# Kernel optimization log

Measured on AMD Instinct MI355X. Metric: run time of the kernel, lower is better.

Reference implementation:

```python
import jax, jax.numpy as jnp
import numpy as np

VOCAB, E, H, B, S, C = 200000, 256, 512, 32, 512, 2


def setup_inputs() -> dict:
    key = jax.random.key(0)
    ks = jax.random.split(key, 10)
    emb = jax.random.normal(ks[0], (VOCAB, E), jnp.float32) * 0.1
    # torch code appends a zero row used as pad_idx
    emb_table = jnp.concatenate([emb, jnp.zeros((1, E), jnp.float32)], axis=0)  # [VOCAB+1, E]
    x = jax.random.randint(ks[1], (B, S), -1, VOCAB, dtype=jnp.int32)  # -1 marks UNK tokens
    unk_vec = jax.random.normal(ks[2], (E,), jnp.float32)
    induction = jax.random.normal(ks[3], (E, E), jnp.float32) / np.float32(np.sqrt(E))
    s = np.float32(1.0 / np.sqrt(H))  # torch GRU default init: U(-1/sqrt(H), 1/sqrt(H))
    W_ih = jax.random.uniform(ks[4], (3 * H, E), jnp.float32, -s, s)
    W_hh = jax.random.uniform(ks[5], (3 * H, H), jnp.float32, -s, s)
    b_ih = jax.random.uniform(ks[6], (3 * H,), jnp.float32, -s, s)
    b_hh = jax.random.uniform(ks[7], (3 * H,), jnp.float32, -s, s)
    W_proj = jax.random.normal(ks[8], (C, H), jnp.float32) * np.float32(np.sqrt(2.0 / (C + H)))  # xavier normal
    b_proj = jnp.zeros((C,), jnp.float32)
    return dict(x=x, emb_table=emb_table, unk_vec=unk_vec, induction=induction,
                W_ih=W_ih, W_hh=W_hh, b_ih=b_ih, b_hh=b_hh, W_proj=W_proj, b_proj=b_proj)


def _gru(e, W_ih, W_hh, b_ih, b_hh):
    # e: [B,S,E] -> hidden states [B,S,H], torch GRU gate order (r, z, n)
    xi = jnp.einsum('bse,ge->bsg', e, W_ih) + b_ih  # precompute input gates, g = 3H
    h0 = jnp.zeros((e.shape[0], W_hh.shape[1]), e.dtype)

    def step(h, xt):
        gh = h @ W_hh.T + b_hh
        xr, xz, xn = jnp.split(xt, 3, axis=-1)
        hr, hz, hn = jnp.split(gh, 3, axis=-1)
        r = jax.nn.sigmoid(xr + hr)
        z = jax.nn.sigmoid(xz + hz)
        n = jnp.tanh(xn + r * hn)
        h_new = (1.0 - z) * n + z * h
        return h_new, h_new

    _, hs = jax.lax.scan(step, h0, jnp.swapaxes(xi, 0, 1))  # [S,B,H]
    return jnp.swapaxes(hs, 0, 1)


def reference(x, emb_table, unk_vec, induction, W_ih, W_hh, b_ih, b_hh, W_proj, b_proj):
    pad_idx = emb_table.shape[0] - 1
    unk = x == -1  # [B,S]
    tok = jnp.where(unk, pad_idx, x)
    e = emb_table[tok]  # [B,S,E] gather (memory-bound)
    # Faithful to induce_embeddings as written: context list is always empty (bug),
    # so every UNK position gets induction_matrix @ unk_vec.
    induced = induction @ unk_vec  # [E]
    e = jnp.where(unk[..., None], induced, e)
    h = _gru(e, W_ih, W_hh, b_ih, b_hh)  # [B,S,H]
    pooled = jnp.max(h, axis=1)  # torch.max(x, 1).values
    # dropout is identity at inference
    return pooled @ W_proj.T + b_proj  # [B,C]
```

## Files before the change

### kernel.cpp

```cpp
#include <hip/hip_runtime.h>
#include <hip/hip_bf16.h>

#define EDIM 256
#define HDIM 512
#define BB 32
#define SS 512
#define CC 2
#define G3 1536

typedef unsigned int u32;
typedef unsigned long long u64;
typedef __attribute__((ext_vector_type(8))) short short8;
typedef __attribute__((ext_vector_type(4))) float f32x4;

__device__ __forceinline__ float toF(float v) { return v; }
__device__ __forceinline__ float toF(__hip_bfloat16 v) { return __bfloat162float(v); }
__device__ __forceinline__ void storeX(float* p, float v) { *p = v; }
__device__ __forceinline__ void storeX(__hip_bfloat16* p, float v) { *p = __float2bfloat16(v); }

__device__ __forceinline__ unsigned short f2bf(float f) {
  u32 b = __float_as_uint(f);
  return (unsigned short)((b + 0x7FFFu + ((b >> 16) & 1u)) >> 16);
}

__global__ void k_init(const float* __restrict__ induction, const float* __restrict__ unk_vec,
                       float* __restrict__ induced, u64* __restrict__ thw) {
  const int t = threadIdx.x;
  const int wg = blockIdx.x;
  if (wg < 16) {
    u64* p = thw + (size_t)wg * 1024;
    for (int i = t; i < 1024; i += 256) p[i] = 0ull;
  } else {
    float acc = 0.f;
    const float* row = induction + t * EDIM;
#pragma unroll 4
    for (int j = 0; j < EDIM; j += 4) {
      float4 a = *(const float4*)(row + j);
      float4 u = *(const float4*)(unk_vec + j);
      acc += a.x * u.x + a.y * u.y + a.z * u.z + a.w * u.w;
    }
    induced[t] = acc;
  }
}

template <typename XT>
__global__ __launch_bounds__(256) void k_xi(const int* __restrict__ x, const float* __restrict__ emb,
                                            const float* __restrict__ induced,
                                            const float* __restrict__ W_ih, const float* __restrict__ b_ih,
                                            XT* __restrict__ xi) {
  __shared__ __align__(16) unsigned short As[128][40];
  __shared__ __align__(16) unsigned short Bs[128][40];
  __shared__ int toks[128];
  __shared__ float bcol[128];
  const int c0 = blockIdx.x * 128;
  const int r0 = blockIdx.y * 128;
  const int tid = threadIdx.x;
  if (tid < 128) { toks[tid] = x[r0 + tid]; bcol[tid] = b_ih[c0 + tid]; }
  __syncthreads();

  const int wv = tid >> 6, ln = tid & 63;
  const int lr = tid & 127, kh = tid >> 7;
  const int fm = ln & 15, fq = ln >> 4;

  f32x4 acc[2][8];
#pragma unroll
  for (int i = 0; i < 2; i++)
#pragma unroll
    for (int j = 0; j < 8; j++) acc[i][j] = (f32x4){0.f, 0.f, 0.f, 0.f};

  const int tok = toks[lr];
  const float* abase = (tok < 0 ? induced : emb + (size_t)tok * EDIM) + kh * 16;
  const float* bbase = W_ih + (size_t)(c0 + lr) * EDIM + kh * 16;

  for (int kk = 0; kk < EDIM; kk += 32) {
    unsigned short av[16], bv[16];
#pragma unroll
    for (int q = 0; q < 4; q++) {
      float4 ta = *(const float4*)(abase + kk + q * 4);
      float4 tb = *(const float4*)(bbase + kk + q * 4);
      av[q * 4 + 0] = f2bf(ta.x); av[q * 4 + 1] = f2bf(ta.y);
      av[q * 4 + 2] = f2bf(ta.z); av[q * 4 + 3] = f2bf(ta.w);
      bv[q * 4 + 0] = f2bf(tb.x); bv[q * 4 + 1] = f2bf(tb.y);
      bv[q * 4 + 2] = f2bf(tb.z); bv[q * 4 + 3] = f2bf(tb.w);
    }
    *(uint4*)&As[lr][kh * 16 + 0] = *(uint4*)&av[0];
    *(uint4*)&As[lr][kh * 16 + 8] = *(uint4*)&av[8];
    *(uint4*)&Bs[lr][kh * 16 + 0] = *(uint4*)&bv[0];
    *(uint4*)&Bs[lr][kh * 16 + 8] = *(uint4*)&bv[8];
    __syncthreads();

    short8 af0 = *(const short8*)&As[wv * 32 + fm][fq * 8];
    short8 af1 = *(const short8*)&As[wv * 32 + 16 + fm][fq * 8];
#pragma unroll
    for (int ni = 0; ni < 8; ni++) {
      short8 bf = *(const short8*)&Bs[ni * 16 + fm][fq * 8];
      acc[0][ni] = __builtin_amdgcn_mfma_f32_16x16x32_bf16(af0, bf, acc[0][ni], 0, 0, 0);
      acc[1][ni] = __builtin_amdgcn_mfma_f32_16x16x32_bf16(af1, bf, acc[1][ni], 0, 0, 0);
    }
    __syncthreads();
  }

#pragma unroll
  for (int mi = 0; mi < 2; mi++)
#pragma unroll
    for (int ni = 0; ni < 8; ni++) {
      const int col = c0 + ni * 16 + fm;
      const float bb = bcol[ni * 16 + fm];
#pragma unroll
      for (int r = 0; r < 4; r++) {
        const int row = r0 + wv * 32 + mi * 16 + fq * 4 + r;
        storeX(xi + (size_t)row * G3 + col, acc[mi][ni][r] + bb);
      }
    }
}

template <typename XT>
__global__ __launch_bounds__(256, 1) void k_gru(const XT* __restrict__ xi, const float* __restrict__ W_hh,
                                                const float* __restrict__ b_hh, u64* __restrict__ thw,
                                                float* __restrict__ pooled) {
  const int wg = blockIdx.x;
  const int g = wg & 7;
  const int m = wg >> 3;
  const int bbase = g * 4;
  const int i0 = m * 16;
  const int tid = threadIdx.x;
  const int iu = tid >> 4;
  const int ks = tid & 15;
  const int i = i0 + iu;
  const int swz = ks & 7;

  f32x4 w[3][8];
#pragma unroll
  for (int q = 0; q < 3; q++) {
    const float* wr = W_hh + (size_t)(q * HDIM + i) * HDIM + ks * 32;
#pragma unroll
    for (int j = 0; j < 8; j++) w[q][j] = *(const f32x4*)(wr + j * 4);
  }
  const float bh0 = b_hh[i], bh1 = b_hh[HDIM + i], bh2 = b_hh[2 * HDIM + i];

  const bool gate = (ks < 4);
  const int gb = ks & 3;
  const int hpIdx = ((((i >> 2) ^ ((i >> 5) & 7)) << 2) | (i & 3));
  const int foff = ((((tid >> 1) ^ ((tid >> 4) & 7)) << 2) | ((tid & 1) << 1));

  u64* slot = thw + (size_t)g * 2 * 1024;
  __shared__ __align__(16) float hs[2][4][512];

  float pmax = -3.0e38f;

  float cxr = 0.f, cxz = 0.f, cxn = 0.f;
  if (gate) {
    const size_t xo = (size_t)(bbase + gb) * SS * G3 + i;
    cxr = toF(xi[xo]); cxz = toF(xi[xo + HDIM]); cxn = toF(xi[xo + 2 * HDIM]);
  }

  for (int s = 0; s < SS; s++) {
    float nxr = 0.f, nxz = 0.f, nxn = 0.f;
    if (gate && s + 1 < SS) {
      const size_t xo = ((size_t)(bbase + gb) * SS + (s + 1)) * G3 + i;
      nxr = toF(xi[xo]); nxz = toF(xi[xo + HDIM]); nxn = toF(xi[xo + 2 * HDIM]);
    }

    float* hb = &hs[s & 1][0][0];
    if (s == 0) {
#pragma unroll
      for (int t = 0; t < 8; t++) hb[t * 256 + tid] = 0.f;
    } else {
      const u64* src = slot + (size_t)(s & 1) * 1024 + tid;
      const u32 need = (u32)s;
      u64 v[4];
#pragma unroll
      for (int j = 0; j < 4; j++)
        v[j] = __hip_atomic_load(src + j * 256, __ATOMIC_RELAXED, __HIP_MEMORY_SCOPE_AGENT);
      u32 pend = 0;
#pragma unroll
      for (int j = 0; j < 4; j++)
        if ((u32)(v[j] & 0xFFFFu) != need) pend |= 1u << j;
      int guard = 0;
      while (pend && guard < (1 << 20)) {
        __builtin_amdgcn_s_sleep(1);
#pragma unroll
        for (int j = 0; j < 4; j++)
          if (pend & (1u << j))
            v[j] = __hip_atomic_load(src + j * 256, __ATOMIC_RELAXED, __HIP_MEMORY_SCOPE_AGENT);
#pragma unroll
        for (int j = 0; j < 4; j++)
          if ((pend & (1u << j)) && (u32)(v[j] & 0xFFFFu) == need) pend &= ~(1u << j);
        guard++;
      }
#pragma unroll
      for (int j = 0; j < 4; j++) {
        const float a = __uint_as_float((u32)(v[j] >> 40) << 8);
        const float b = __uint_as_float((u32)((v[j] >> 16) & 0xFFFFFFu) << 8);
        *(float2*)&hb[j * 512 + foff] = make_float2(a, b);
      }
    }
    __syncthreads();

    f32x4 acc[4][3];
#pragma unroll
    for (int b = 0; b < 4; b++)
#pragma unroll
      for (int q = 0; q < 3; q++) acc[b][q] = (f32x4){0.f, 0.f, 0.f, 0.f};

#pragma unroll
    for (int b = 0; b < 4; b++) {
      const float* hr = hb + b * 512 + ks * 32;
#pragma unroll
      for (int j = 0; j < 8; j++) {
        const f32x4 hv = *(const f32x4*)(hr + ((j ^ swz) << 2));
        acc[b][0] = __builtin_elementwise_fma(w[0][j], hv, acc[b][0]);
        acc[b][1] = __builtin_elementwise_fma(w[1][j], hv, acc[b][1]);
        acc[b][2] = __builtin_elementwise_fma(w[2][j], hv, acc[b][2]);
      }
    }

    float ha[4][3];
#pragma unroll
    for (int b = 0; b < 4; b++)
#pragma unroll
      for (int q = 0; q < 3; q++) {
        const f32x4 t = acc[b][q];
        ha[b][q] = (t.x + t.y) + (t.z + t.w);
      }

    float v3[3];
#pragma unroll
    for (int q = 0; q < 3; q++) {
      const float s01 = (ks & 1) ? ha[0][q] : ha[1][q];
      const float r01 = __shfl_xor(s01, 1, 64);
      const float k01 = (ks & 1) ? ha[1][q] : ha[0][q];
      const float a01 = k01 + r01;
      const float s23 = (ks & 1) ? ha[2][q] : ha[3][q];
      const float r23 = __shfl_xor(s23, 1, 64);
      const float k23 = (ks & 1) ? ha[3][q] : ha[2][q];
      const float a23 = k23 + r23;
      const float s2 = (ks & 2) ? a01 : a23;
      const float r2 = __shfl_xor(s2, 2, 64);
      const float k2 = (ks & 2) ? a23 : a01;
      float t = k2 + r2;
      t += __shfl_xor(t, 4, 64);
      t += __shfl_xor(t, 8, 64);
      v3[q] = t;
    }

    if (gate) {
      const float hr_ = bh0 + v3[0];
      const float hz_ = bh1 + v3[1];
      const float hn_ = bh2 + v3[2];
      const float r = 1.f / (1.f + expf(-(cxr + hr_)));
      const float z = 1.f / (1.f + expf(-(cxz + hz_)));
      const float n = tanhf(cxn + r * hn_);
      const float hp = hb[gb * 512 + hpIdx];
      const float hnew = (1.f - z) * n + z * hp;
      pmax = fmaxf(pmax, hnew);
      const float pv = __shfl_xor(hnew, 16, 64);
      if (!(iu & 1)) {
        const u32 abits = ((__float_as_uint(hnew) + 0x80u) >> 8) & 0xFFFFFFu;
        const u32 bbits = ((__float_as_uint(pv) + 0x80u) >> 8) & 0xFFFFFFu;
        const u64 pkt = ((u64)abits << 40) | ((u64)bbits << 16) | (u64)(u32)(s + 1);
        const int W = gb * 256 + (i >> 1);
        __hip_atomic_store(slot + (size_t)((s + 1) & 1) * 1024 + W, pkt,
                           __ATOMIC_RELAXED, __HIP_MEMORY_SCOPE_AGENT);
      }
    }
    cxr = nxr; cxz = nxz; cxn = nxn;
  }

  if (gate) pooled[(size_t)(bbase + gb) * HDIM + i] = pmax;
}

__global__ void k_out(const float* __restrict__ pooled, const float* __restrict__ W_proj,
                      const float* __restrict__ b_proj, float* __restrict__ out) {
  const int t = threadIdx.x;
  const int b = t >> 1, c = t & 1;
  const float* p = pooled + (size_t)b * HDIM;
  const float* wr = W_proj + (size_t)c * HDIM;
  float acc = 0.f;
#pragma unroll 4
  for (int k = 0; k < HDIM; k += 4) {
    float4 pv = *(const float4*)(p + k);
    float4 wv = *(const float4*)(wr + k);
    acc += pv.x * wv.x + pv.y * wv.y + pv.z * wv.z + pv.w * wv.w;
  }
  out[b * CC + c] = acc + b_proj[c];
}

extern "C" void kernel_launch(void* const* d_in, const int* in_sizes, int n_in,
                              void* d_out, int out_size, void* d_ws, size_t ws_size,
                              hipStream_t stream) {
  const int* x = (const int*)d_in[0];
  const float* emb = (const float*)d_in[1];
  const float* unk = (const float*)d_in[2];
  const float* induction = (const float*)d_in[3];
  const float* W_ih = (const float*)d_in[4];
  const float* W_hh = (const float*)d_in[5];
  const float* b_ih = (const float*)d_in[6];
  const float* b_hh = (const float*)d_in[7];
  const float* W_proj = (const float*)d_in[8];
  const float* b_proj = (const float*)d_in[9];
  float* out = (float*)d_out;

  const size_t xi_f32 = (size_t)BB * SS * G3 * 4;
  const size_t xi_b16 = (size_t)BB * SS * G3 * 2;
  const size_t thw_sz = (size_t)8 * 2 * 1024 * 8;
  const size_t tail = thw_sz + (size_t)BB * HDIM * 4 + EDIM * 4 + 4096;
  const bool usef32 = ws_size >= xi_f32 + tail;

  char* p = (char*)d_ws;
  void* xi = p;
  p += ((usef32 ? xi_f32 : xi_b16) + 255) & ~(size_t)255;
  u64* thw = (u64*)p;         p += thw_sz;
  float* pooled = (float*)p;  p += (size_t)BB * HDIM * 4;
  float* induced = (float*)p;

  k_init<<<17, 256, 0, stream>>>(induction, unk, induced, thw);
  if (usef32) {
    k_xi<float><<<dim3(12, 128), 256, 0, stream>>>(x, emb, induced, W_ih, b_ih, (float*)xi);
    k_gru<float><<<256, 256, 0, stream>>>((const float*)xi, W_hh, b_hh, thw, pooled);
  } else {
    k_xi<__hip_bfloat16><<<dim3(12, 128), 256, 0, stream>>>(x, emb, induced, W_ih, b_ih,
                                                            (__hip_bfloat16*)xi);
    k_gru<__hip_bfloat16><<<256, 256, 0, stream>>>((const __hip_bfloat16*)xi, W_hh, b_hh, thw, pooled);
  }
  k_out<<<1, 64, 0, stream>>>(pooled, W_proj, b_proj, out);
}
```

Baseline: 1.781 ms.

## Split each GRU step into two batch-pair phases to overlap cross-workgroup waits

Each workgroup's four batch rows are processed as two pairs per timestep. Each pair waits only on its own two slots of the previous hidden state, then runs its matvec, gate math and publish before the second pair starts. This lets compute for one pair overlap with the arrival of the other pair's data from peer workgroups. The cost is an extra __syncthreads per step, a shorter polling guard, and more serialized per-step phases, which could lengthen the critical path.

```diff
diff --git a/kernel.cpp b/kernel.cpp
--- a/kernel.cpp
+++ b/kernel.cpp
@@ -138,136 +138,140 @@
   }
   const float bh0 = b_hh[i], bh1 = b_hh[HDIM + i], bh2 = b_hh[2 * HDIM + i];
 
-  const bool gate = (ks < 4);
-  const int gb = ks & 3;
+  const bool gate = (ks < 2);
   const int hpIdx = ((((i >> 2) ^ ((i >> 5) & 7)) << 2) | (i & 3));
   const int foff = ((((tid >> 1) ^ ((tid >> 4) & 7)) << 2) | ((tid & 1) << 1));
 
   u64* slot = thw + (size_t)g * 2 * 1024;
   __shared__ __align__(16) float hs[2][4][512];
 
-  float pmax = -3.0e38f;
-
-  float cxr = 0.f, cxz = 0.f, cxn = 0.f;
+  float pmax[2] = {-3.0e38f, -3.0e38f};
+
+  float cx[2][3] = {{0.f, 0.f, 0.f}, {0.f, 0.f, 0.f}};
   if (gate) {
-    const size_t xo = (size_t)(bbase + gb) * SS * G3 + i;
-    cxr = toF(xi[xo]); cxz = toF(xi[xo + HDIM]); cxn = toF(xi[xo + 2 * HDIM]);
+#pragma unroll
+    for (int P = 0; P < 2; P++) {
+      const size_t xo = (size_t)(bbase + 2 * P + ks) * SS * G3 + i;
+      cx[P][0] = toF(xi[xo]); cx[P][1] = toF(xi[xo + HDIM]); cx[P][2] = toF(xi[xo + 2 * HDIM]);
+    }
   }
 
   for (int s = 0; s < SS; s++) {
-    float nxr = 0.f, nxz = 0.f, nxn = 0.f;
+    float nx[2][3] = {{0.f, 0.f, 0.f}, {0.f, 0.f, 0.f}};
     if (gate && s + 1 < SS) {
-      const size_t xo = ((size_t)(bbase + gb) * SS + (s + 1)) * G3 + i;
-      nxr = toF(xi[xo]); nxz = toF(xi[xo + HDIM]); nxn = toF(xi[xo + 2 * HDIM]);
+#pragma unroll
+      for (int P = 0; P < 2; P++) {
+        const size_t xo = ((size_t)(bbase + 2 * P + ks) * SS + (s + 1)) * G3 + i;
+        nx[P][0] = toF(xi[xo]); nx[P][1] = toF(xi[xo + HDIM]); nx[P][2] = toF(xi[xo + 2 * HDIM]);
+      }
     }
 
     float* hb = &hs[s & 1][0][0];
-    if (s == 0) {
-#pragma unroll
-      for (int t = 0; t < 8; t++) hb[t * 256 + tid] = 0.f;
-    } else {
-      const u64* src = slot + (size_t)(s & 1) * 1024 + tid;
-      const u32 need = (u32)s;
-      u64 v[4];
-#pragma unroll
-      for (int j = 0; j < 4; j++)
-        v[j] = __hip_atomic_load(src + j * 256, __ATOMIC_RELAXED, __HIP_MEMORY_SCOPE_AGENT);
-      u32 pend = 0;
-#pragma unroll
-      for (int j = 0; j < 4; j++)
-        if ((u32)(v[j] & 0xFFFFu) != need) pend |= 1u << j;
-      int guard = 0;
-      while (pend && guard < (1 << 20)) {
-        __builtin_amdgcn_s_sleep(1);
-#pragma unroll
-        for (int j = 0; j < 4; j++)
-          if (pend & (1u << j))
-            v[j] = __hip_atomic_load(src + j * 256, __ATOMIC_RELAXED, __HIP_MEMORY_SCOPE_AGENT);
-#pragma unroll
-        for (int j = 0; j < 4; j++)
-          if ((pend & (1u << j)) && (u32)(v[j] & 0xFFFFu) == need) pend &= ~(1u << j);
-        guard++;
-      }
-#pragma unroll
-      for (int j = 0; j < 4; j++) {
-        const float a = __uint_as_float((u32)(v[j] >> 40) << 8);
-        const float b = __uint_as_float((u32)((v[j] >> 16) & 0xFFFFFFu) << 8);
-        *(float2*)&hb[j * 512 + foff] = make_float2(a, b);
-      }
-    }
-    __syncthreads();
-
-    f32x4 acc[4][3];
-#pragma unroll
-    for (int b = 0; b < 4; b++)
-#pragma unroll
-      for (int q = 0; q < 3; q++) acc[b][q] = (f32x4){0.f, 0.f, 0.f, 0.f};
-
-#pragma unroll
-    for (int b = 0; b < 4; b++) {
-      const float* hr = hb + b * 512 + ks * 32;
-#pragma unroll
-      for (int j = 0; j < 8; j++) {
-        const f32x4 hv = *(const f32x4*)(hr + ((j ^ swz) << 2));
-        acc[b][0] = __builtin_elementwise_fma(w[0][j], hv, acc[b][0]);
-        acc[b][1] = __builtin_elementwise_fma(w[1][j], hv, acc[b][1]);
-        acc[b][2] = __builtin_elementwise_fma(w[2][j], hv, acc[b][2]);
-      }
-    }
-
-    float ha[4][3];
-#pragma unroll
-    for (int b = 0; b < 4; b++)
+
+#pragma unroll
+    for (int P = 0; P < 2; P++) {
+      if (s == 0) {
+        if (P == 0) {
+#pragma unroll
+          for (int t = 0; t < 8; t++) hb[t * 256 + tid] = 0.f;
+        }
+      } else {
+        const u32 need = (u32)s;
+        const u64* src = slot + (size_t)(s & 1) * 1024 + 2 * P * 256 + tid;
+        u64 v0 = __hip_atomic_load(src, __ATOMIC_RELAXED, __HIP_MEMORY_SCOPE_AGENT);
+        u64 v1 = __hip_atomic_load(src + 256, __ATOMIC_RELAXED, __HIP_MEMORY_SCOPE_AGENT);
+        int guard = 0;
+        while ((((u32)(v0 & 0xFFFFu) != need) || ((u32)(v1 & 0xFFFFu) != need)) && guard < (1 << 18)) {
+          __builtin_amdgcn_s_sleep(1);
+          if ((u32)(v0 & 0xFFFFu) != need)
+            v0 = __hip_atomic_load(src, __ATOMIC_RELAXED, __HIP_MEMORY_SCOPE_AGENT);
+          if ((u32)(v1 & 0xFFFFu) != need)
+            v1 = __hip_atomic_load(src + 256, __ATOMIC_RELAXED, __HIP_MEMORY_SCOPE_AGENT);
+          guard++;
+        }
+        {
+          const float a0 = __uint_as_float((u32)(v0 >> 40) << 8);
+          const float b0 = __uint_as_float((u32)((v0 >> 16) & 0xFFFFFFu) << 8);
+          *(float2*)&hb[(2 * P) * 512 + foff] = make_float2(a0, b0);
+          const float a1 = __uint_as_float((u32)(v1 >> 40) << 8);
+          const float b1 = __uint_as_float((u32)((v1 >> 16) & 0xFFFFFFu) << 8);
+          *(float2*)&hb[(2 * P + 1) * 512 + foff] = make_float2(a1, b1);
+        }
+      }
+      __syncthreads();
+
+      f32x4 acc[2][3];
+#pragma unroll
+      for (int b = 0; b < 2; b++)
+#pragma unroll
+        for (int q = 0; q < 3; q++) acc[b][q] = (f32x4){0.f, 0.f, 0.f, 0.f};
+
+#pragma unroll
+      for (int b = 0; b < 2; b++) {
+        const float* hr = hb + (2 * P + b) * 512 + ks * 32;
+#pragma unroll
+        for (int j = 0; j < 8; j++) {
+          const f32x4 hv = *(const f32x4*)(hr + ((j ^ swz) << 2));
+          acc[b][0] = __builtin_elementwise_fma(w[0][j], hv, acc[b][0]);
+          acc[b][1] = __builtin_elementwise_fma(w[1][j], hv, acc[b][1]);
+          acc[b][2] = __builtin_elementwise_fma(w[2][j], hv, acc[b][2]);
+        }
+      }
+
+      float ha[2][3];
+#pragma unroll
+      for (int b = 0; b < 2; b++)
+#pragma unroll
+        for (int q = 0; q < 3; q++) {
+          const f32x4 t = acc[b][q];
+          ha[b][q] = (t.x + t.y) + (t.z + t.w);
+        }
+
+      float v3[3];
 #pragma unroll
       for (int q = 0; q < 3; q++) {
-        const f32x4 t = acc[b][q];
-        ha[b][q] = (t.x + t.y) + (t.z + t.w);
-      }
-
-    float v3[3];
-#pragma unroll
-    for (int q = 0; q < 3; q++) {
-      const float s01 = (ks & 1) ? ha[0][q] : ha[1][q];
-      const float r01 = __shfl_xor(s01, 1, 64);
-      const float k01 = (ks & 1) ? ha[1][q] : ha[0][q];
-      const float a01 = k01 + r01;
-      const float s23 = (ks & 1) ? ha[2][q] : ha[3][q];
-      const float r23 = __shfl_xor(s23, 1, 64);
-      const float k23 = (ks & 1) ? ha[3][q] : ha[2][q];
-      const float a23 = k23 + r23;
-      const float s2 = (ks & 2) ? a01 : a23;
-      const float r2 = __shfl_xor(s2, 2, 64);
-      const float k2 = (ks & 2) ? a23 : a01;
-      float t = k2 + r2;
-      t += __shfl_xor(t, 4, 64);
-      t += __shfl_xor(t, 8, 64);
-      v3[q] = t;
-    }
-
-    if (gate) {
-      const float hr_ = bh0 + v3[0];
-      const float hz_ = bh1 + v3[1];
-      const float hn_ = bh2 + v3[2];
-      const float r = 1.f / (1.f + expf(-(cxr + hr_)));
-      const float z = 1.f / (1.f + expf(-(cxz + hz_)));
-      const float n = tanhf(cxn + r * hn_);
-      const float hp = hb[gb * 512 + hpIdx];
-      const float hnew = (1.f - z) * n + z * hp;
-      pmax = fmaxf(pmax, hnew);
-      const float pv = __shfl_xor(hnew, 16, 64);
-      if (!(iu & 1)) {
-        const u32 abits = ((__float_as_uint(hnew) + 0x80u) >> 8) & 0xFFFFFFu;
-        const u32 bbits = ((__float_as_uint(pv) + 0x80u) >> 8) & 0xFFFFFFu;
-        const u64 pkt = ((u64)abits << 40) | ((u64)bbits << 16) | (u64)(u32)(s + 1);
-        const int W = gb * 256 + (i >> 1);
-        __hip_atomic_store(slot + (size_t)((s + 1) & 1) * 1024 + W, pkt,
-                           __ATOMIC_RELAXED, __HIP_MEMORY_SCOPE_AGENT);
-      }
-    }
-    cxr = nxr; cxz = nxz; cxn = nxn;
-  }
-
-  if (gate) pooled[(size_t)(bbase + gb) * HDIM + i] = pmax;
+        const float s01 = (ks & 1) ? ha[0][q] : ha[1][q];
+        const float r01 = __shfl_xor(s01, 1, 64);
+        const float k01 = (ks & 1) ? ha[1][q] : ha[0][q];
+        float t = k01 + r01;
+        t += __shfl_xor(t, 2, 64);
+        t += __shfl_xor(t, 4, 64);
+        t += __shfl_xor(t, 8, 64);
+        v3[q] = t;
+      }
+
+      if (gate) {
+        const float hr_ = bh0 + v3[0];
+        const float hz_ = bh1 + v3[1];
+        const float hn_ = bh2 + v3[2];
+        const float r = 1.f / (1.f + expf(-(cx[P][0] + hr_)));
+        const float z = 1.f / (1.f + expf(-(cx[P][1] + hz_)));
+        const float n = tanhf(cx[P][2] + r * hn_);
+        const float hp = hb[(2 * P + ks) * 512 + hpIdx];
+        const float hnew = (1.f - z) * n + z * hp;
+        pmax[P] = fmaxf(pmax[P], hnew);
+        const float pv = __shfl_xor(hnew, 16, 64);
+        if (!(iu & 1)) {
+          const u32 abits = ((__float_as_uint(hnew) + 0x80u) >> 8) & 0xFFFFFFu;
+          const u32 bbits = ((__float_as_uint(pv) + 0x80u) >> 8) & 0xFFFFFFu;
+          const u64 pkt = ((u64)abits << 40) | ((u64)bbits << 16) | (u64)(u32)(s + 1);
+          const int W = (2 * P + ks) * 256 + (i >> 1);
+          __hip_atomic_store(slot + (size_t)((s + 1) & 1) * 1024 + W, pkt,
+                             __ATOMIC_RELAXED, __HIP_MEMORY_SCOPE_AGENT);
+        }
+      }
+    }
+
+#pragma unroll
+    for (int P = 0; P < 2; P++) {
+      cx[P][0] = nx[P][0]; cx[P][1] = nx[P][1]; cx[P][2] = nx[P][2];
+    }
+  }
+
+  if (gate) {
+    pooled[(size_t)(bbase + ks) * HDIM + i] = pmax[0];
+    pooled[(size_t)(bbase + 2 + ks) * HDIM + i] = pmax[1];
+  }
 }
 
 __global__ void k_out(const float* __restrict__ pooled, const float* __restrict__ W_proj,
```

Result: no change. 1.783 ms (+0.1%).
